# Kernel tuning notes

Hardware: AMD Instinct MI355X
Metric: run time of the kernel (lower is better)

Reference implementation:

```python
import jax, jax.numpy as jnp
import numpy as np
import math

NUM_HEADS = 8


def setup_inputs() -> dict:
    key = jax.random.key(0)
    ks = jax.random.split(key, 6)
    b, s, e = 4, 2048, 512
    x = jax.random.normal(ks[0], (b, s, e), dtype=jnp.float32)
    # 0/1 adjacency matrix as float (it multiplies the scores in the module)
    adj = jax.random.randint(ks[1], (b, s, s), 0, 2).astype(jnp.float32)
    scale = 0.02
    Wqkv_w = jax.random.normal(ks[2], (3 * e, e), dtype=jnp.float32) * scale
    Wqkv_b = jax.random.normal(ks[3], (3 * e,), dtype=jnp.float32) * scale
    out_w = jax.random.normal(ks[4], (e, e), dtype=jnp.float32) * scale
    out_b = jax.random.normal(ks[5], (e,), dtype=jnp.float32) * scale
    return {"x": x, "adj": adj, "Wqkv_w": Wqkv_w, "Wqkv_b": Wqkv_b,
            "out_w": out_w, "out_b": out_b}


def reference(x, adj, Wqkv_w, Wqkv_b, out_w, out_b):
    b, s, e = x.shape
    h = NUM_HEADS
    d = e // h
    # fused qkv projection: (b, s, 3*e) -> (b, s, 3, h, d)
    qkv = (x @ Wqkv_w.T + Wqkv_b).reshape(b, s, 3, h, d)
    qkv = jnp.transpose(qkv, (2, 0, 3, 1, 4))  # (3, b, h, s, d)
    q, k, v = qkv[0], qkv[1], qkv[2]
    inv_sqrt_d = 1.0 / math.sqrt(d)
    scores = jnp.einsum('bhqd,bhkd->bhqk', q, k) * inv_sqrt_d
    scores = jnp.clip(scores * adj[:, None, :, :], -10000.0, 10000.0)
    attn = jax.nn.softmax(scores, axis=-1)
    out = jnp.einsum('bhqk,bhkd->bhqd', attn, v)
    out = jnp.transpose(out, (0, 2, 1, 3)).reshape(b, s, e)  # (b, s, h*d)
    return out @ out_w.T + out_b
```

## Files before the change

kernel.cpp:

```cpp
#include <hip/hip_runtime.h>


typedef __attribute__((ext_vector_type(8))) short bf16x8;
typedef __attribute__((ext_vector_type(4))) float f32x4;
typedef __attribute__((ext_vector_type(4))) unsigned short ushort4v;
typedef __attribute__((ext_vector_type(4))) _Float16 f16x4;
typedef __attribute__((ext_vector_type(8))) _Float16 f16x8;
typedef __attribute__((ext_vector_type(2))) __fp16 h16x2;

#if __has_builtin(__builtin_amdgcn_exp2f)
#define EXP2F(x) __builtin_amdgcn_exp2f(x)
#else
#define EXP2F(x) exp2f(x)
#endif

#define QSCALE 0.18033688011112042f

__device__ __forceinline__ unsigned short f2bf(float f) {
  unsigned int u = __float_as_uint(f);
  u += 0x7FFFu + ((u >> 16) & 1u);
  return (unsigned short)(u >> 16);
}
__device__ __forceinline__ unsigned short f2h(float f) {
  union { _Float16 h; unsigned short u; } cv;
  cv.h = (_Float16)f;
  return cv.u;
}

__device__ __forceinline__ int sbit(unsigned w, int pos) {
  return ((int)(w << (31 - pos))) >> 31;
}

__device__ __forceinline__ f16x8 pk8(const float* p) {
  union { struct { h16x2 a, b, c, d; } s; f16x8 v; } u;
  u.s.a = __builtin_amdgcn_cvt_pkrtz(p[0], p[1]);
  u.s.b = __builtin_amdgcn_cvt_pkrtz(p[2], p[3]);
  u.s.c = __builtin_amdgcn_cvt_pkrtz(p[4], p[5]);
  u.s.d = __builtin_amdgcn_cvt_pkrtz(p[6], p[7]);
  return u.v;
}

__device__ __forceinline__ f32x4 mfma_pv(f16x8 a, f16x8 b, f32x4 c) {
#if __has_builtin(__builtin_amdgcn_mfma_f32_16x16x32_f16)
  return __builtin_amdgcn_mfma_f32_16x16x32_f16(a, b, c, 0, 0, 0);
#else
  union { f16x8 v; struct { f16x4 lo, hi; } s; } ua, ub;
  ua.v = a; ub.v = b;
  c = __builtin_amdgcn_mfma_f32_16x16x16f16(ua.s.lo, ub.s.lo, c, 0, 0, 0);
  return __builtin_amdgcn_mfma_f32_16x16x16f16(ua.s.hi, ub.s.hi, c, 0, 0, 0);
#endif
}

__global__ __launch_bounds__(256) void prep_k(const float* __restrict__ x,
                                              unsigned short* __restrict__ x_bf,
                                              const float* __restrict__ wqkv,
                                              unsigned short* __restrict__ wqkv_bf,
                                              const float* __restrict__ outw,
                                              unsigned short* __restrict__ outw_bf,
                                              const float* __restrict__ adj,
                                              unsigned long long* __restrict__ abits) {
  const int bid = blockIdx.x;
  if (bid < 5120) {
    const float* in; unsigned short* out; int i;
    if (bid < 4096) { in = x; out = x_bf; i = bid * 256 + threadIdx.x; }
    else if (bid < 4864) { in = wqkv; out = wqkv_bf; i = (bid - 4096) * 256 + threadIdx.x; }
    else { in = outw; out = outw_bf; i = (bid - 4864) * 256 + threadIdx.x; }
    float4 v = ((const float4*)in)[i];
    ushort4v o;
    o[0] = f2bf(v.x); o[1] = f2bf(v.y); o[2] = f2bf(v.z); o[3] = f2bf(v.w);
    ((ushort4v*)out)[i] = o;
  } else {
    const int gw = (bid - 5120) * 4 + (threadIdx.x >> 6);
    const int l = threadIdx.x & 63;
    const int b = gw >> 11, q = gw & 2047;
    const float* row = adj + ((size_t)b * 2048 + q) * 2048;
    unsigned long long* ob = abits + (size_t)b * 65536 + q;
#pragma unroll 4
    for (int kt = 0; kt < 32; ++kt) {
      const float v = row[kt * 64 + l];
      const unsigned long long m = __ballot(v != 0.f);
      if (l == 0) ob[(size_t)kt * 2048] = m;
    }
  }
}

template <int MODE>
__global__ __launch_bounds__(256, 3) void gemm128_k(const unsigned short* __restrict__ A,
                                                    const unsigned short* __restrict__ Bt,
                                                    const float* __restrict__ bias, int Kdim,
                                                    int Ntiles, unsigned short* __restrict__ q_out,
                                                    unsigned short* __restrict__ k_out,
                                                    unsigned short* __restrict__ v_out,
                                                    float* __restrict__ f_out) {
  __shared__ union {
    struct { unsigned short A[2][128][40], B[2][128][40]; } s;
    unsigned short T[64][136];
  } u;

  const int t = threadIdx.x;
  const int lane = t & 63, w = t >> 6, ln = lane & 15, quad = lane >> 4;
  const int xcd = blockIdx.x & 7, loc = blockIdx.x >> 3;
  const int mt = xcd * ((gridDim.x >> 3) / Ntiles) + loc / Ntiles;
  const int nt = loc % Ntiles;
  const int wm = (w >> 1) * 64, wn = (w & 1) * 64;
  const int strow = t >> 2, stcol = (t & 3) * 8;

  const size_t abase = (size_t)(mt * 128 + strow) * Kdim + stcol;
  const size_t bbase = (size_t)(nt * 128 + strow) * Kdim + stcol;

  f32x4 acc[4][4];
#pragma unroll
  for (int i = 0; i < 4; ++i)
#pragma unroll
    for (int j = 0; j < 4; ++j) acc[i][j] = (f32x4){0.f, 0.f, 0.f, 0.f};

  bf16x8 a0 = *(const bf16x8*)(A + abase);
  bf16x8 a1 = *(const bf16x8*)(A + abase + (size_t)64 * Kdim);
  bf16x8 b0 = *(const bf16x8*)(Bt + bbase);
  bf16x8 b1 = *(const bf16x8*)(Bt + bbase + (size_t)64 * Kdim);
  *(bf16x8*)&u.s.A[0][strow][stcol] = a0;
  *(bf16x8*)&u.s.A[0][64 + strow][stcol] = a1;
  *(bf16x8*)&u.s.B[0][strow][stcol] = b0;
  *(bf16x8*)&u.s.B[0][64 + strow][stcol] = b1;
  __syncthreads();

  const int iters = Kdim >> 5;
  for (int it = 0; it < iters; ++it) {
    const int cur = it & 1, nxt = cur ^ 1;

    const int kn = ((it + 1) << 5) & (Kdim - 1);
    a0 = *(const bf16x8*)(A + abase + kn);
    a1 = *(const bf16x8*)(A + abase + (size_t)64 * Kdim + kn);
    b0 = *(const bf16x8*)(Bt + bbase + kn);
    b1 = *(const bf16x8*)(Bt + bbase + (size_t)64 * Kdim + kn);

    bf16x8 bfr[4];
#pragma unroll
    for (int nf = 0; nf < 4; ++nf)
      bfr[nf] = *(const bf16x8*)&u.s.B[cur][wn + nf * 16 + ln][quad * 8];
#pragma unroll
    for (int mf = 0; mf < 4; ++mf) {
      bf16x8 af = *(const bf16x8*)&u.s.A[cur][wm + mf * 16 + ln][quad * 8];
#pragma unroll
      for (int nf = 0; nf < 4; ++nf)
        acc[mf][nf] = __builtin_amdgcn_mfma_f32_16x16x32_bf16(af, bfr[nf], acc[mf][nf], 0, 0, 0);
    }

    if (it + 1 < iters) {
      *(bf16x8*)&u.s.A[nxt][strow][stcol] = a0;
      *(bf16x8*)&u.s.A[nxt][64 + strow][stcol] = a1;
      *(bf16x8*)&u.s.B[nxt][strow][stcol] = b0;
      *(bf16x8*)&u.s.B[nxt][64 + strow][stcol] = b1;
      __syncthreads();
    }
  }

  if (MODE == 0 && nt >= 8) {
    const int bb = mt >> 4, sq0 = (mt & 15) * 128;
#pragma unroll
    for (int half = 0; half < 2; ++half) {
      __syncthreads();
      if ((w & 1) == half) {
#pragma unroll
        for (int nf = 0; nf < 4; ++nf) {
          const float bv = bias[nt * 128 + half * 64 + nf * 16 + ln];
#pragma unroll
          for (int mf = 0; mf < 4; ++mf)
#pragma unroll
            for (int r = 0; r < 4; ++r)
              u.T[nf * 16 + ln][wm + mf * 16 + quad * 4 + r] = f2h(acc[mf][nf][r] + bv);
        }
      }
      __syncthreads();
#pragma unroll
      for (int rep = 0; rep < 4; ++rep) {
        const int row = rep * 16 + (t >> 4), c = t & 15;
        const bf16x8 val = *(const bf16x8*)&u.T[row][c * 8];
        const int hd = (nt - 8) * 128 + half * 64 + row;
        const int hh = hd >> 6, dd = hd & 63;
        *(bf16x8*)(v_out + ((size_t)(bb * 8 + hh) * 64 + dd) * 2048 + sq0 + c * 8) = val;
      }
    }
    return;
  }

#pragma unroll
  for (int mf = 0; mf < 4; ++mf) {
    const int m = mt * 128 + wm + mf * 16 + quad * 4;
#pragma unroll
    for (int nf = 0; nf < 4; ++nf) {
      const int n = nt * 128 + wn + nf * 16 + ln;
      const float bv = bias[n];
      if (MODE == 0) {
        const int hd = n & 511;
        const int hh = hd >> 6, dd = hd & 63;
        const int bb = m >> 11, sq = m & 2047;
        if (n < 512) {
#pragma unroll
          for (int r = 0; r < 4; ++r)
            q_out[((size_t)(bb * 8 + hh) * 2048 + sq + r) * 64 + dd] =
                f2bf((acc[mf][nf][r] + bv) * QSCALE);
        } else {
#pragma unroll
          for (int r = 0; r < 4; ++r)
            k_out[((size_t)(bb * 8 + hh) * 2048 + sq + r) * 64 + dd] = f2bf(acc[mf][nf][r] + bv);
        }
      } else {
#pragma unroll
        for (int r = 0; r < 4; ++r) f_out[(size_t)(m + r) * 512 + n] = acc[mf][nf][r] + bv;
      }
    }
  }
}

__global__ __launch_bounds__(256, 2) void attn_k(const unsigned short* __restrict__ Qg,
                                                 const unsigned short* __restrict__ Kg,
                                                 const unsigned short* __restrict__ Vg,
                                                 const unsigned long long* __restrict__ Mg,
                                                 unsigned short* __restrict__ Og) {
  __shared__ unsigned short K_lds[2][64][64];
  __shared__ unsigned short V_lds[2][64][64];
  __shared__ unsigned long long M_lds[2][128];

  const int t = threadIdx.x;
  const int w = t >> 6, lane = t & 63, ln = lane & 15, quad = lane >> 4;
  const int bh = blockIdx.x & 31, qt = blockIdx.x >> 5, bb = bh >> 3;
  const int sbase = qt * 128;

  const unsigned short* Qp = Qg + (size_t)bh * (2048 * 64);
  const unsigned short* Kp = Kg + (size_t)bh * (2048 * 64);
  const unsigned short* Vp = Vg + (size_t)bh * (64 * 2048);
  const unsigned long long* Mp = Mg + (size_t)bb * 65536 + sbase;

  bf16x8 qf[2][2];
#pragma unroll
  for (int qg = 0; qg < 2; ++qg) {
    const int qrow = sbase + w * 32 + qg * 16 + ln;
    qf[qg][0] = *(const bf16x8*)(Qp + (size_t)qrow * 64 + quad * 8);
    qf[qg][1] = *(const bf16x8*)(Qp + (size_t)qrow * 64 + 32 + quad * 8);
  }

  const _Float16 one_h = (_Float16)((ln == 0) ? 1.0f : 0.0f);
  const f16x8 vf_one = (f16x8){one_h, one_h, one_h, one_h, one_h, one_h, one_h, one_h};

  f32x4 acc_o[2][4];
#pragma unroll
  for (int qg = 0; qg < 2; ++qg)
#pragma unroll
    for (int dg = 0; dg < 4; ++dg) acc_o[qg][dg] = (f32x4){0.f, 0.f, 0.f, 0.f};
  f32x4 acc_1[2] = {(f32x4){0.f, 0.f, 0.f, 0.f}, (f32x4){0.f, 0.f, 0.f, 0.f}};

  const int strow = t >> 2;
  const int stcol = (t & 3) * 16;
  const int c0 = (t & 3) * 2;
  const int gkw = (strow & 3) | (((strow >> 3) & 1) << 2);
  const int gvw = strow & 7;

  const unsigned short* Kl = Kp + (size_t)strow * 64 + stcol;
  const unsigned short* Vl = Vp + (size_t)strow * 2048 + stcol;

  bf16x8 kr0 = *(const bf16x8*)(Kl);
  bf16x8 kr1 = *(const bf16x8*)(Kl + 8);
  bf16x8 vr0 = *(const bf16x8*)(Vl);
  bf16x8 vr1 = *(const bf16x8*)(Vl + 8);
  unsigned long long mreg = (w < 2) ? Mp[w * 64 + lane] : 0ull;
  *(bf16x8*)&K_lds[0][strow][(c0 ^ gkw) << 3] = kr0;
  *(bf16x8*)&K_lds[0][strow][((c0 + 1) ^ gkw) << 3] = kr1;
  *(bf16x8*)&V_lds[0][strow][(c0 ^ gvw) << 3] = vr0;
  *(bf16x8*)&V_lds[0][strow][((c0 + 1) ^ gvw) << 3] = vr1;
  if (w < 2) M_lds[0][w * 64 + lane] = mreg;
  __syncthreads();

  const int mq = w * 32 + ln;
  const int kperm = ((ln >> 2) << 3) + (ln & 3);
  const int gkr = (ln & 3) | (((ln >> 2) & 1) << 2);
  const int gvr = ln & 7;

  for (int kt = 0; kt < 32; ++kt) {
    const int cur = kt & 1, nxt = cur ^ 1;

    kr0 = *(const bf16x8*)(Kl + (size_t)(kt + 1) * 4096);
    kr1 = *(const bf16x8*)(Kl + (size_t)(kt + 1) * 4096 + 8);
    vr0 = *(const bf16x8*)(Vl + (kt + 1) * 64);
    vr1 = *(const bf16x8*)(Vl + (kt + 1) * 64 + 8);
    mreg = (w < 2) ? Mp[(size_t)(kt + 1) * 2048 + w * 64 + lane] : 0ull;

    f32x4 sc[2][4];
#pragma unroll
    for (int h = 0; h < 2; ++h)
#pragma unroll
      for (int e = 0; e < 2; ++e) {
        const int krow = h * 32 + kperm + e * 4;
        const int kc = (quad ^ gkr) << 3;
        bf16x8 kf0 = *(const bf16x8*)&K_lds[cur][krow][kc];
        bf16x8 kf1 = *(const bf16x8*)&K_lds[cur][krow][kc ^ 32];
#pragma unroll
        for (int qg = 0; qg < 2; ++qg) {
          f32x4 z = (f32x4){0.f, 0.f, 0.f, 0.f};
          z = __builtin_amdgcn_mfma_f32_16x16x32_bf16(kf0, qf[qg][0], z, 0, 0, 0);
          sc[qg][h * 2 + e] = __builtin_amdgcn_mfma_f32_16x16x32_bf16(kf1, qf[qg][1], z, 0, 0, 0);
        }
      }

    f16x8 vfa[2][4];
#pragma unroll
    for (int h = 0; h < 2; ++h)
#pragma unroll
      for (int dg = 0; dg < 4; ++dg)
        vfa[h][dg] = *(const f16x8*)&V_lds[cur][dg * 16 + ln][((h * 4 + quad) ^ gvr) << 3];

    f16x8 pa[2][2];
#pragma unroll
    for (int qg = 0; qg < 2; ++qg) {
      const unsigned long long m64 = M_lds[cur][mq + qg * 16];
#pragma unroll
      for (int h = 0; h < 2; ++h) {
        const unsigned wrd = (h ? (unsigned)(m64 >> 32) : (unsigned)m64) >> (quad * 8);
        float p[8];
#pragma unroll
        for (int e = 0; e < 2; ++e)
#pragma unroll
          for (int r = 0; r < 4; ++r) {
            const int j = e * 4 + r;
            const int se = sbit(wrd, j);
            const float s = __int_as_float(__float_as_int(sc[qg][h * 2 + e][r]) & se);
            p[j] = EXP2F(s);
          }
        pa[qg][h] = pk8(p);
      }
    }

#pragma unroll
    for (int h = 0; h < 2; ++h)
#pragma unroll
      for (int qg = 0; qg < 2; ++qg) {
#pragma unroll
        for (int dg = 0; dg < 4; ++dg)
          acc_o[qg][dg] = mfma_pv(pa[qg][h], vfa[h][dg], acc_o[qg][dg]);
        acc_1[qg] = mfma_pv(pa[qg][h], vf_one, acc_1[qg]);
      }

    if (kt < 31) {
      *(bf16x8*)&K_lds[nxt][strow][(c0 ^ gkw) << 3] = kr0;
      *(bf16x8*)&K_lds[nxt][strow][((c0 + 1) ^ gkw) << 3] = kr1;
      *(bf16x8*)&V_lds[nxt][strow][(c0 ^ gvw) << 3] = vr0;
      *(bf16x8*)&V_lds[nxt][strow][((c0 + 1) ^ gvw) << 3] = vr1;
      if (w < 2) M_lds[nxt][w * 64 + lane] = mreg;
      __syncthreads();
    }
  }

  unsigned short* Op = Og + (size_t)bb * 2048 * 512 + (size_t)(bh & 7) * 64;
#pragma unroll
  for (int qg = 0; qg < 2; ++qg)
#pragma unroll
    for (int r = 0; r < 4; ++r) {
      const float inv = 1.0f / __shfl(acc_1[qg][r], quad * 16);
      const int sq = sbase + w * 32 + qg * 16 + quad * 4 + r;
#pragma unroll
      for (int dg = 0; dg < 4; ++dg)
        Op[(size_t)sq * 512 + dg * 16 + ln] = f2bf(acc_o[qg][dg][r] * inv);
    }
}

extern "C" void kernel_launch(void* const* d_in, const int* in_sizes, int n_in, void* d_out,
                              int out_size, void* d_ws, size_t ws_size, hipStream_t stream) {
  const float* x = (const float*)d_in[0];
  const float* adj = (const float*)d_in[1];
  const float* wqkv = (const float*)d_in[2];
  const float* bqkv = (const float*)d_in[3];
  const float* outw = (const float*)d_in[4];
  const float* outb = (const float*)d_in[5];
  float* out = (float*)d_out;

  char* ws = (char*)d_ws;
  unsigned short* x_bf = (unsigned short*)(ws);
  unsigned short* wqkv_bf = (unsigned short*)(ws + 8388608);
  unsigned short* outw_bf = (unsigned short*)(ws + 9961472);
  unsigned long long* abits = (unsigned long long*)(ws + 10485760);
  unsigned short* Qb = (unsigned short*)(ws + 27262976);
  unsigned short* Kb = (unsigned short*)(ws + 35651584);
  unsigned short* Vb = (unsigned short*)(ws + 44040192);
  unsigned short* Ob = (unsigned short*)(ws + 52428800);

  prep_k<<<7168, 256, 0, stream>>>(x, x_bf, wqkv, wqkv_bf, outw, outw_bf, adj, abits);

  gemm128_k<0><<<768, 256, 0, stream>>>(x_bf, wqkv_bf, bqkv, 512, 12, Qb, Kb, Vb, nullptr);

  attn_k<<<512, 256, 0, stream>>>(Qb, Kb, Vb, abits, Ob);

  gemm128_k<1><<<256, 256, 0, stream>>>(Ob, outw_bf, outb, 512, 4, nullptr, nullptr, nullptr, out);
}
```

Before: 211.2 us.

## Use two waves per attention block with 64 query rows per wave

The attention kernel now launches 128 threads (2 waves) per block instead of 4, and each wave handles 64 query rows (4 query groups) instead of 32. Each K/V fragment read from LDS is therefore reused across twice as many MFMAs, which cuts LDS traffic per FLOP. Each thread also stages twice as much K/V per tile. The cost is much higher register pressure from 4x4 accumulators and unroll 2, plus fewer waves per block and launch_bounds(128,1), so latency hiding and occupancy may suffer.

```diff
diff --git a/kernel.cpp b/kernel.cpp
--- a/kernel.cpp
+++ b/kernel.cpp
@@ -213,7 +213,7 @@
   }
 }
 
-__global__ __launch_bounds__(256, 2) void attn_k(const unsigned short* __restrict__ Qg,
+__global__ __launch_bounds__(128, 1) void attn_k(const unsigned short* __restrict__ Qg,
                                                  const unsigned short* __restrict__ Kg,
                                                  const unsigned short* __restrict__ Vg,
                                                  const unsigned long long* __restrict__ Mg,
@@ -232,10 +232,10 @@
   const unsigned short* Vp = Vg + (size_t)bh * (64 * 2048);
   const unsigned long long* Mp = Mg + (size_t)bb * 65536 + sbase;
 
-  bf16x8 qf[2][2];
-#pragma unroll
-  for (int qg = 0; qg < 2; ++qg) {
-    const int qrow = sbase + w * 32 + qg * 16 + ln;
+  bf16x8 qf[4][2];
+#pragma unroll
+  for (int qg = 0; qg < 4; ++qg) {
+    const int qrow = sbase + w * 64 + qg * 16 + ln;
     qf[qg][0] = *(const bf16x8*)(Qp + (size_t)qrow * 64 + quad * 8);
     qf[qg][1] = *(const bf16x8*)(Qp + (size_t)qrow * 64 + 32 + quad * 8);
   }
@@ -243,16 +243,18 @@
   const _Float16 one_h = (_Float16)((ln == 0) ? 1.0f : 0.0f);
   const f16x8 vf_one = (f16x8){one_h, one_h, one_h, one_h, one_h, one_h, one_h, one_h};
 
-  f32x4 acc_o[2][4];
-#pragma unroll
-  for (int qg = 0; qg < 2; ++qg)
+  f32x4 acc_o[4][4];
+#pragma unroll
+  for (int qg = 0; qg < 4; ++qg)
 #pragma unroll
     for (int dg = 0; dg < 4; ++dg) acc_o[qg][dg] = (f32x4){0.f, 0.f, 0.f, 0.f};
-  f32x4 acc_1[2] = {(f32x4){0.f, 0.f, 0.f, 0.f}, (f32x4){0.f, 0.f, 0.f, 0.f}};
-
-  const int strow = t >> 2;
-  const int stcol = (t & 3) * 16;
-  const int c0 = (t & 3) * 2;
+  f32x4 acc_1[4];
+#pragma unroll
+  for (int qg = 0; qg < 4; ++qg) acc_1[qg] = (f32x4){0.f, 0.f, 0.f, 0.f};
+
+  const int strow = t >> 1;
+  const int stcol = (t & 1) * 32;
+  const int c0 = (t & 1) * 4;
   const int gkw = (strow & 3) | (((strow >> 3) & 1) << 2);
   const int gvw = strow & 7;
 
@@ -261,41 +263,54 @@
 
   bf16x8 kr0 = *(const bf16x8*)(Kl);
   bf16x8 kr1 = *(const bf16x8*)(Kl + 8);
+  bf16x8 kr2 = *(const bf16x8*)(Kl + 16);
+  bf16x8 kr3 = *(const bf16x8*)(Kl + 24);
   bf16x8 vr0 = *(const bf16x8*)(Vl);
   bf16x8 vr1 = *(const bf16x8*)(Vl + 8);
-  unsigned long long mreg = (w < 2) ? Mp[w * 64 + lane] : 0ull;
-  *(bf16x8*)&K_lds[0][strow][(c0 ^ gkw) << 3] = kr0;
+  bf16x8 vr2 = *(const bf16x8*)(Vl + 16);
+  bf16x8 vr3 = *(const bf16x8*)(Vl + 24);
+  unsigned long long mreg = Mp[t];
+  *(bf16x8*)&K_lds[0][strow][((c0 + 0) ^ gkw) << 3] = kr0;
   *(bf16x8*)&K_lds[0][strow][((c0 + 1) ^ gkw) << 3] = kr1;
-  *(bf16x8*)&V_lds[0][strow][(c0 ^ gvw) << 3] = vr0;
+  *(bf16x8*)&K_lds[0][strow][((c0 + 2) ^ gkw) << 3] = kr2;
+  *(bf16x8*)&K_lds[0][strow][((c0 + 3) ^ gkw) << 3] = kr3;
+  *(bf16x8*)&V_lds[0][strow][((c0 + 0) ^ gvw) << 3] = vr0;
   *(bf16x8*)&V_lds[0][strow][((c0 + 1) ^ gvw) << 3] = vr1;
-  if (w < 2) M_lds[0][w * 64 + lane] = mreg;
+  *(bf16x8*)&V_lds[0][strow][((c0 + 2) ^ gvw) << 3] = vr2;
+  *(bf16x8*)&V_lds[0][strow][((c0 + 3) ^ gvw) << 3] = vr3;
+  M_lds[0][t] = mreg;
   __syncthreads();
 
-  const int mq = w * 32 + ln;
+  const int mq = w * 64 + ln;
   const int kperm = ((ln >> 2) << 3) + (ln & 3);
   const int gkr = (ln & 3) | (((ln >> 2) & 1) << 2);
   const int gvr = ln & 7;
-
+  const int kc = (quad ^ gkr) << 3;
+
+#pragma unroll 2
   for (int kt = 0; kt < 32; ++kt) {
     const int cur = kt & 1, nxt = cur ^ 1;
 
     kr0 = *(const bf16x8*)(Kl + (size_t)(kt + 1) * 4096);
     kr1 = *(const bf16x8*)(Kl + (size_t)(kt + 1) * 4096 + 8);
+    kr2 = *(const bf16x8*)(Kl + (size_t)(kt + 1) * 4096 + 16);
+    kr3 = *(const bf16x8*)(Kl + (size_t)(kt + 1) * 4096 + 24);
     vr0 = *(const bf16x8*)(Vl + (kt + 1) * 64);
     vr1 = *(const bf16x8*)(Vl + (kt + 1) * 64 + 8);
-    mreg = (w < 2) ? Mp[(size_t)(kt + 1) * 2048 + w * 64 + lane] : 0ull;
-
-    f32x4 sc[2][4];
+    vr2 = *(const bf16x8*)(Vl + (kt + 1) * 64 + 16);
+    vr3 = *(const bf16x8*)(Vl + (kt + 1) * 64 + 24);
+    mreg = Mp[(size_t)(kt + 1) * 2048 + t];
+
+    f32x4 sc[4][4];
 #pragma unroll
     for (int h = 0; h < 2; ++h)
 #pragma unroll
       for (int e = 0; e < 2; ++e) {
         const int krow = h * 32 + kperm + e * 4;
-        const int kc = (quad ^ gkr) << 3;
         bf16x8 kf0 = *(const bf16x8*)&K_lds[cur][krow][kc];
         bf16x8 kf1 = *(const bf16x8*)&K_lds[cur][krow][kc ^ 32];
 #pragma unroll
-        for (int qg = 0; qg < 2; ++qg) {
+        for (int qg = 0; qg < 4; ++qg) {
           f32x4 z = (f32x4){0.f, 0.f, 0.f, 0.f};
           z = __builtin_amdgcn_mfma_f32_16x16x32_bf16(kf0, qf[qg][0], z, 0, 0, 0);
           sc[qg][h * 2 + e] = __builtin_amdgcn_mfma_f32_16x16x32_bf16(kf1, qf[qg][1], z, 0, 0, 0);
@@ -309,9 +324,9 @@
       for (int dg = 0; dg < 4; ++dg)
         vfa[h][dg] = *(const f16x8*)&V_lds[cur][dg * 16 + ln][((h * 4 + quad) ^ gvr) << 3];
 
-    f16x8 pa[2][2];
-#pragma unroll
-    for (int qg = 0; qg < 2; ++qg) {
+    f16x8 pa[4][2];
+#pragma unroll
+    for (int qg = 0; qg < 4; ++qg) {
       const unsigned long long m64 = M_lds[cur][mq + qg * 16];
 #pragma unroll
       for (int h = 0; h < 2; ++h) {
@@ -333,7 +348,7 @@
 #pragma unroll
     for (int h = 0; h < 2; ++h)
 #pragma unroll
-      for (int qg = 0; qg < 2; ++qg) {
+      for (int qg = 0; qg < 4; ++qg) {
 #pragma unroll
         for (int dg = 0; dg < 4; ++dg)
           acc_o[qg][dg] = mfma_pv(pa[qg][h], vfa[h][dg], acc_o[qg][dg]);
@@ -341,22 +356,26 @@
       }
 
     if (kt < 31) {
-      *(bf16x8*)&K_lds[nxt][strow][(c0 ^ gkw) << 3] = kr0;
+      *(bf16x8*)&K_lds[nxt][strow][((c0 + 0) ^ gkw) << 3] = kr0;
       *(bf16x8*)&K_lds[nxt][strow][((c0 + 1) ^ gkw) << 3] = kr1;
-      *(bf16x8*)&V_lds[nxt][strow][(c0 ^ gvw) << 3] = vr0;
+      *(bf16x8*)&K_lds[nxt][strow][((c0 + 2) ^ gkw) << 3] = kr2;
+      *(bf16x8*)&K_lds[nxt][strow][((c0 + 3) ^ gkw) << 3] = kr3;
+      *(bf16x8*)&V_lds[nxt][strow][((c0 + 0) ^ gvw) << 3] = vr0;
       *(bf16x8*)&V_lds[nxt][strow][((c0 + 1) ^ gvw) << 3] = vr1;
-      if (w < 2) M_lds[nxt][w * 64 + lane] = mreg;
+      *(bf16x8*)&V_lds[nxt][strow][((c0 + 2) ^ gvw) << 3] = vr2;
+      *(bf16x8*)&V_lds[nxt][strow][((c0 + 3) ^ gvw) << 3] = vr3;
+      M_lds[nxt][t] = mreg;
       __syncthreads();
     }
   }
 
   unsigned short* Op = Og + (size_t)bb * 2048 * 512 + (size_t)(bh & 7) * 64;
 #pragma unroll
-  for (int qg = 0; qg < 2; ++qg)
+  for (int qg = 0; qg < 4; ++qg)
 #pragma unroll
     for (int r = 0; r < 4; ++r) {
       const float inv = 1.0f / __shfl(acc_1[qg][r], quad * 16);
-      const int sq = sbase + w * 32 + qg * 16 + quad * 4 + r;
+      const int sq = sbase + w * 64 + qg * 16 + quad * 4 + r;
 #pragma unroll
       for (int dg = 0; dg < 4; ++dg)
         Op[(size_t)sq * 512 + dg * 16 + ln] = f2bf(acc_o[qg][dg][r] * inv);
@@ -387,7 +406,7 @@
 
   gemm128_k<0><<<768, 256, 0, stream>>>(x_bf, wqkv_bf, bqkv, 512, 12, Qb, Kb, Vb, nullptr);
 
-  attn_k<<<512, 256, 0, stream>>>(Qb, Kb, Vb, abits, Ob);
+  attn_k<<<512, 128, 0, stream>>>(Qb, Kb, Vb, abits, Ob);
 
   gemm128_k<1><<<256, 256, 0, stream>>>(Ob, outw_bf, outb, 512, 4, nullptr, nullptr, nullptr, out);
 }
```

Result: slower. 235.2 us (+11.3%).

## Split attention key range in two and merge partial outputs

Applied to the files above, without the earlier changes.

The attention kernel now splits the 2048 keys into two halves, doubling the grid from 512 to 1024 blocks. Each block writes unnormalized fp16 partial outputs and fp32 row sums, which a new merge kernel adds and normalizes into the bf16 attention output. The aim is better occupancy across the GPU's compute units, since 512 blocks underfill the device. In exchange it adds an extra launch plus a partial-output round trip through memory (staged in the output buffer), and the unnormalized fp16 partials could lose precision or overflow.

```diff
diff --git a/kernel.cpp b/kernel.cpp
--- a/kernel.cpp
+++ b/kernel.cpp
@@ -217,20 +217,22 @@
                                                  const unsigned short* __restrict__ Kg,
                                                  const unsigned short* __restrict__ Vg,
                                                  const unsigned long long* __restrict__ Mg,
-                                                 unsigned short* __restrict__ Og) {
+                                                 unsigned short* __restrict__ Od,
+                                                 float* __restrict__ Lp) {
   __shared__ unsigned short K_lds[2][64][64];
   __shared__ unsigned short V_lds[2][64][64];
   __shared__ unsigned long long M_lds[2][128];
 
   const int t = threadIdx.x;
   const int w = t >> 6, lane = t & 63, ln = lane & 15, quad = lane >> 4;
-  const int bh = blockIdx.x & 31, qt = blockIdx.x >> 5, bb = bh >> 3;
+  const int blk = blockIdx.x;
+  const int bh = blk & 31, qt = (blk >> 5) & 15, sp = blk >> 9, bb = bh >> 3;
   const int sbase = qt * 128;
 
   const unsigned short* Qp = Qg + (size_t)bh * (2048 * 64);
-  const unsigned short* Kp = Kg + (size_t)bh * (2048 * 64);
-  const unsigned short* Vp = Vg + (size_t)bh * (64 * 2048);
-  const unsigned long long* Mp = Mg + (size_t)bb * 65536 + sbase;
+  const unsigned short* Kp = Kg + (size_t)bh * (2048 * 64) + (size_t)sp * (1024 * 64);
+  const unsigned short* Vp = Vg + (size_t)bh * (64 * 2048) + (size_t)sp * 1024;
+  const unsigned long long* Mp = Mg + (size_t)bb * 65536 + sbase + (size_t)sp * (16 * 2048);
 
   bf16x8 qf[2][2];
 #pragma unroll
@@ -276,7 +278,7 @@
   const int gkr = (ln & 3) | (((ln >> 2) & 1) << 2);
   const int gvr = ln & 7;
 
-  for (int kt = 0; kt < 32; ++kt) {
+  for (int kt = 0; kt < 16; ++kt) {
     const int cur = kt & 1, nxt = cur ^ 1;
 
     kr0 = *(const bf16x8*)(Kl + (size_t)(kt + 1) * 4096);
@@ -340,7 +342,7 @@
         acc_1[qg] = mfma_pv(pa[qg][h], vf_one, acc_1[qg]);
       }
 
-    if (kt < 31) {
+    if (kt < 15) {
       *(bf16x8*)&K_lds[nxt][strow][(c0 ^ gkw) << 3] = kr0;
       *(bf16x8*)&K_lds[nxt][strow][((c0 + 1) ^ gkw) << 3] = kr1;
       *(bf16x8*)&V_lds[nxt][strow][(c0 ^ gvw) << 3] = vr0;
@@ -350,17 +352,38 @@
     }
   }
 
-  unsigned short* Op = Og + (size_t)bb * 2048 * 512 + (size_t)(bh & 7) * 64;
+  unsigned short* Opp = Od + (size_t)sp * (4 * 2048 * 512) +
+                        (size_t)bb * (2048 * 512) + (size_t)(bh & 7) * 64;
+  float* Lpp = Lp + (size_t)sp * 65536 + (size_t)bh * 2048;
 #pragma unroll
   for (int qg = 0; qg < 2; ++qg)
 #pragma unroll
     for (int r = 0; r < 4; ++r) {
-      const float inv = 1.0f / __shfl(acc_1[qg][r], quad * 16);
       const int sq = sbase + w * 32 + qg * 16 + quad * 4 + r;
+      if (ln == 0) Lpp[sq] = acc_1[qg][r];
 #pragma unroll
       for (int dg = 0; dg < 4; ++dg)
-        Op[(size_t)sq * 512 + dg * 16 + ln] = f2bf(acc_o[qg][dg][r] * inv);
-    }
+        Opp[(size_t)sq * 512 + dg * 16 + ln] = f2h(acc_o[qg][dg][r]);
+    }
+}
+
+__global__ __launch_bounds__(256) void merge_k(const unsigned short* __restrict__ Op,
+                                               const float* __restrict__ Lp,
+                                               unsigned short* __restrict__ Ob) {
+  const int t = threadIdx.x;
+  const int row = blockIdx.x * 4 + (t >> 6);
+  const int e0 = (t & 63) * 8;
+  const int b = row >> 11, s = row & 2047, h = e0 >> 6;
+  const int li = (b * 8 + h) * 2048 + s;
+  const float inv = 1.0f / (Lp[li] + Lp[65536 + li]);
+  union { f16x8 v; } o0, o1;
+  o0.v = *(const f16x8*)(Op + (size_t)row * 512 + e0);
+  o1.v = *(const f16x8*)(Op + (size_t)(4 * 2048 * 512) + (size_t)row * 512 + e0);
+  union { bf16x8 v; unsigned short u[8]; } out;
+#pragma unroll
+  for (int j = 0; j < 8; ++j)
+    out.u[j] = f2bf(((float)o0.v[j] + (float)o1.v[j]) * inv);
+  *(bf16x8*)(Ob + (size_t)row * 512 + e0) = out.v;
 }
 
 extern "C" void kernel_launch(void* const* d_in, const int* in_sizes, int n_in, void* d_out,
@@ -378,16 +401,20 @@
   unsigned short* wqkv_bf = (unsigned short*)(ws + 8388608);
   unsigned short* outw_bf = (unsigned short*)(ws + 9961472);
   unsigned long long* abits = (unsigned long long*)(ws + 10485760);
+  float* Lsum = (float*)(ws + 12582912);
   unsigned short* Qb = (unsigned short*)(ws + 27262976);
   unsigned short* Kb = (unsigned short*)(ws + 35651584);
   unsigned short* Vb = (unsigned short*)(ws + 44040192);
   unsigned short* Ob = (unsigned short*)(ws + 52428800);
+  unsigned short* Opart = (unsigned short*)d_out;
 
   prep_k<<<7168, 256, 0, stream>>>(x, x_bf, wqkv, wqkv_bf, outw, outw_bf, adj, abits);
 
   gemm128_k<0><<<768, 256, 0, stream>>>(x_bf, wqkv_bf, bqkv, 512, 12, Qb, Kb, Vb, nullptr);
 
-  attn_k<<<512, 256, 0, stream>>>(Qb, Kb, Vb, abits, Ob);
+  attn_k<<<1024, 256, 0, stream>>>(Qb, Kb, Vb, abits, Opart, Lsum);
+
+  merge_k<<<2048, 256, 0, stream>>>(Opart, Lsum, Ob);
 
   gemm128_k<1><<<256, 256, 0, stream>>>(Ob, outw_bf, outb, 512, 4, nullptr, nullptr, nullptr, out);
 }
```

Result: slower. 221.2 us (+4.7%).

## Split attention key tile across wave pairs and reduce partial outputs in LDS

Applied to the files above, without the earlier changes.

The attention kernel now gives each wave 64 query rows and half of each 64-key tile, instead of 32 query rows and the whole tile. Each wave's K fragment loads are reused across four query groups, so fewer LDS reads happen per MFMA. The two key-half partial accumulators and row sums are combined through new shared buffers at the end. This adds about 35KB of LDS and more accumulator registers per wave, which may reduce occupancy under the two-blocks-per-SM launch bound.

```diff
diff --git a/kernel.cpp b/kernel.cpp
--- a/kernel.cpp
+++ b/kernel.cpp
@@ -221,9 +221,12 @@
   __shared__ unsigned short K_lds[2][64][64];
   __shared__ unsigned short V_lds[2][64][64];
   __shared__ unsigned long long M_lds[2][128];
+  __shared__ float Rf[128][68];
+  __shared__ float Rl[128];
 
   const int t = threadIdx.x;
   const int w = t >> 6, lane = t & 63, ln = lane & 15, quad = lane >> 4;
+  const int wq = w & 1, wk = w >> 1;
   const int bh = blockIdx.x & 31, qt = blockIdx.x >> 5, bb = bh >> 3;
   const int sbase = qt * 128;
 
@@ -232,10 +235,10 @@
   const unsigned short* Vp = Vg + (size_t)bh * (64 * 2048);
   const unsigned long long* Mp = Mg + (size_t)bb * 65536 + sbase;
 
-  bf16x8 qf[2][2];
-#pragma unroll
-  for (int qg = 0; qg < 2; ++qg) {
-    const int qrow = sbase + w * 32 + qg * 16 + ln;
+  bf16x8 qf[4][2];
+#pragma unroll
+  for (int qg = 0; qg < 4; ++qg) {
+    const int qrow = sbase + wq * 64 + qg * 16 + ln;
     qf[qg][0] = *(const bf16x8*)(Qp + (size_t)qrow * 64 + quad * 8);
     qf[qg][1] = *(const bf16x8*)(Qp + (size_t)qrow * 64 + 32 + quad * 8);
   }
@@ -243,12 +246,14 @@
   const _Float16 one_h = (_Float16)((ln == 0) ? 1.0f : 0.0f);
   const f16x8 vf_one = (f16x8){one_h, one_h, one_h, one_h, one_h, one_h, one_h, one_h};
 
-  f32x4 acc_o[2][4];
-#pragma unroll
-  for (int qg = 0; qg < 2; ++qg)
+  f32x4 acc_o[4][4];
+#pragma unroll
+  for (int qg = 0; qg < 4; ++qg)
 #pragma unroll
     for (int dg = 0; dg < 4; ++dg) acc_o[qg][dg] = (f32x4){0.f, 0.f, 0.f, 0.f};
-  f32x4 acc_1[2] = {(f32x4){0.f, 0.f, 0.f, 0.f}, (f32x4){0.f, 0.f, 0.f, 0.f}};
+  f32x4 acc_1[4];
+#pragma unroll
+  for (int qg = 0; qg < 4; ++qg) acc_1[qg] = (f32x4){0.f, 0.f, 0.f, 0.f};
 
   const int strow = t >> 2;
   const int stcol = (t & 3) * 16;
@@ -271,10 +276,11 @@
   if (w < 2) M_lds[0][w * 64 + lane] = mreg;
   __syncthreads();
 
-  const int mq = w * 32 + ln;
+  const int mq = wq * 64 + ln;
   const int kperm = ((ln >> 2) << 3) + (ln & 3);
   const int gkr = (ln & 3) | (((ln >> 2) & 1) << 2);
   const int gvr = ln & 7;
+  const int kc = (quad ^ gkr) << 3;
 
   for (int kt = 0; kt < 32; ++kt) {
     const int cur = kt & 1, nxt = cur ^ 1;
@@ -285,60 +291,54 @@
     vr1 = *(const bf16x8*)(Vl + (kt + 1) * 64 + 8);
     mreg = (w < 2) ? Mp[(size_t)(kt + 1) * 2048 + w * 64 + lane] : 0ull;
 
-    f32x4 sc[2][4];
-#pragma unroll
-    for (int h = 0; h < 2; ++h)
+    bf16x8 kf[2][2];
+#pragma unroll
+    for (int e = 0; e < 2; ++e) {
+      const int krow = wk * 32 + kperm + e * 4;
+      kf[e][0] = *(const bf16x8*)&K_lds[cur][krow][kc];
+      kf[e][1] = *(const bf16x8*)&K_lds[cur][krow][kc ^ 32];
+    }
+
+    f32x4 sc[4][2];
+#pragma unroll
+    for (int qg = 0; qg < 4; ++qg)
 #pragma unroll
       for (int e = 0; e < 2; ++e) {
-        const int krow = h * 32 + kperm + e * 4;
-        const int kc = (quad ^ gkr) << 3;
-        bf16x8 kf0 = *(const bf16x8*)&K_lds[cur][krow][kc];
-        bf16x8 kf1 = *(const bf16x8*)&K_lds[cur][krow][kc ^ 32];
-#pragma unroll
-        for (int qg = 0; qg < 2; ++qg) {
-          f32x4 z = (f32x4){0.f, 0.f, 0.f, 0.f};
-          z = __builtin_amdgcn_mfma_f32_16x16x32_bf16(kf0, qf[qg][0], z, 0, 0, 0);
-          sc[qg][h * 2 + e] = __builtin_amdgcn_mfma_f32_16x16x32_bf16(kf1, qf[qg][1], z, 0, 0, 0);
+        f32x4 z = (f32x4){0.f, 0.f, 0.f, 0.f};
+        z = __builtin_amdgcn_mfma_f32_16x16x32_bf16(kf[e][0], qf[qg][0], z, 0, 0, 0);
+        sc[qg][e] = __builtin_amdgcn_mfma_f32_16x16x32_bf16(kf[e][1], qf[qg][1], z, 0, 0, 0);
+      }
+
+    f16x8 vfa[4];
+#pragma unroll
+    for (int dg = 0; dg < 4; ++dg)
+      vfa[dg] = *(const f16x8*)&V_lds[cur][dg * 16 + ln][((wk * 4 + quad) ^ gvr) << 3];
+
+    f16x8 pa[4];
+#pragma unroll
+    for (int qg = 0; qg < 4; ++qg) {
+      const unsigned long long m64 = M_lds[cur][mq + qg * 16];
+      const unsigned wrd = (wk ? (unsigned)(m64 >> 32) : (unsigned)m64) >> (quad * 8);
+      float p[8];
+#pragma unroll
+      for (int e = 0; e < 2; ++e)
+#pragma unroll
+        for (int r = 0; r < 4; ++r) {
+          const int j = e * 4 + r;
+          const int se = sbit(wrd, j);
+          const float s = __int_as_float(__float_as_int(sc[qg][e][r]) & se);
+          p[j] = EXP2F(s);
         }
-      }
-
-    f16x8 vfa[2][4];
-#pragma unroll
-    for (int h = 0; h < 2; ++h)
+      pa[qg] = pk8(p);
+    }
+
+#pragma unroll
+    for (int qg = 0; qg < 4; ++qg) {
 #pragma unroll
       for (int dg = 0; dg < 4; ++dg)
-        vfa[h][dg] = *(const f16x8*)&V_lds[cur][dg * 16 + ln][((h * 4 + quad) ^ gvr) << 3];
-
-    f16x8 pa[2][2];
-#pragma unroll
-    for (int qg = 0; qg < 2; ++qg) {
-      const unsigned long long m64 = M_lds[cur][mq + qg * 16];
-#pragma unroll
-      for (int h = 0; h < 2; ++h) {
-        const unsigned wrd = (h ? (unsigned)(m64 >> 32) : (unsigned)m64) >> (quad * 8);
-        float p[8];
-#pragma unroll
-        for (int e = 0; e < 2; ++e)
-#pragma unroll
-          for (int r = 0; r < 4; ++r) {
-            const int j = e * 4 + r;
-            const int se = sbit(wrd, j);
-            const float s = __int_as_float(__float_as_int(sc[qg][h * 2 + e][r]) & se);
-            p[j] = EXP2F(s);
-          }
-        pa[qg][h] = pk8(p);
-      }
-    }
-
-#pragma unroll
-    for (int h = 0; h < 2; ++h)
-#pragma unroll
-      for (int qg = 0; qg < 2; ++qg) {
-#pragma unroll
-        for (int dg = 0; dg < 4; ++dg)
-          acc_o[qg][dg] = mfma_pv(pa[qg][h], vfa[h][dg], acc_o[qg][dg]);
-        acc_1[qg] = mfma_pv(pa[qg][h], vf_one, acc_1[qg]);
-      }
+        acc_o[qg][dg] = mfma_pv(pa[qg], vfa[dg], acc_o[qg][dg]);
+      acc_1[qg] = mfma_pv(pa[qg], vf_one, acc_1[qg]);
+    }
 
     if (kt < 31) {
       *(bf16x8*)&K_lds[nxt][strow][(c0 ^ gkw) << 3] = kr0;
@@ -350,17 +350,33 @@
     }
   }
 
-  unsigned short* Op = Og + (size_t)bb * 2048 * 512 + (size_t)(bh & 7) * 64;
-#pragma unroll
-  for (int qg = 0; qg < 2; ++qg)
-#pragma unroll
-    for (int r = 0; r < 4; ++r) {
-      const float inv = 1.0f / __shfl(acc_1[qg][r], quad * 16);
-      const int sq = sbase + w * 32 + qg * 16 + quad * 4 + r;
-#pragma unroll
-      for (int dg = 0; dg < 4; ++dg)
-        Op[(size_t)sq * 512 + dg * 16 + ln] = f2bf(acc_o[qg][dg][r] * inv);
-    }
+  if (wk == 1) {
+#pragma unroll
+    for (int qg = 0; qg < 4; ++qg)
+#pragma unroll
+      for (int r = 0; r < 4; ++r) {
+        const int q = wq * 64 + qg * 16 + quad * 4 + r;
+        if (ln == 0) Rl[q] = acc_1[qg][r];
+#pragma unroll
+        for (int dg = 0; dg < 4; ++dg) Rf[q][dg * 16 + ln] = acc_o[qg][dg][r];
+      }
+  }
+  __syncthreads();
+  if (wk == 0) {
+    unsigned short* Op = Og + (size_t)bb * 2048 * 512 + (size_t)(bh & 7) * 64;
+#pragma unroll
+    for (int qg = 0; qg < 4; ++qg)
+#pragma unroll
+      for (int r = 0; r < 4; ++r) {
+        const int q = wq * 64 + qg * 16 + quad * 4 + r;
+        const float inv = 1.0f / (__shfl(acc_1[qg][r], quad * 16) + Rl[q]);
+        const int sq = sbase + q;
+#pragma unroll
+        for (int dg = 0; dg < 4; ++dg)
+          Op[(size_t)sq * 512 + dg * 16 + ln] =
+              f2bf((acc_o[qg][dg][r] + Rf[q][dg * 16 + ln]) * inv);
+      }
+  }
 }
 
 extern "C" void kernel_launch(void* const* d_in, const int* in_sizes, int n_in, void* d_out,
```

Result: no change. 214.7 us (+1.6%).
